# Optimization experiments

Hardware: AMD Instinct MI355X
Metric: run time of the kernel (lower is better)

## Reference

```python
import jax, jax.numpy as jnp
import numpy as np

NB = 5  # frequency bands


def _ln(x, g, b, eps=1e-5):
    m = jnp.mean(x, axis=-1, keepdims=True)
    v = jnp.var(x, axis=-1, keepdims=True)
    return (x - m) / jnp.sqrt(v + eps) * g + b


def _graph_adj(x, adj_w, sw1, sb1, sw2, sb2, pos_factor, pos_enc):
    # x: [B, D, N] -> degree-normalized adjacency [B, N, N]
    d = x.shape[1]
    xt = jnp.swapaxes(x, 1, 2)  # [B, N, D]
    # concat-MLP first layer split: cat(xi, xj) @ W1 == xi @ W1[:d] + xj @ W1[d:]
    a = xt @ sw1[:d]
    bpart = xt @ sw1[d:]
    h = jax.nn.elu(a[:, :, None, :] + bpart[:, None, :, :] + sb1)  # [B, N, N, H]
    dyn = jax.nn.sigmoid(jnp.squeeze(h @ sw2, -1) + sb2)  # [B, N, N]
    static = jax.nn.softmax(adj_w, axis=-1)
    pos = jax.nn.softmax(pos_enc, axis=-1)
    comb = jax.nn.softmax(static + dyn + pos_factor * pos, axis=-1)
    deg = jnp.sum(comb, axis=-1)
    dis = (deg + 1e-8) ** -0.5
    return dis[:, :, None] * comb * dis[:, None, :]


def _gcn(x, adj, w, b):
    # x: [B, D, N], adj: [B, N, N] -> [B, D_out, N]
    xt = jnp.swapaxes(x, 1, 2)
    out = jnp.einsum('bij,bjd->bid', adj, xt) @ w + b
    return jnp.swapaxes(out, 1, 2)


def _mha(x, qkv_w, qkv_b, ow, ob, nh=4):
    B, S, D = x.shape
    dh = D // nh
    q, k, v = jnp.split(x @ qkv_w + qkv_b, 3, axis=-1)
    q = q.reshape(B, S, nh, dh)
    k = k.reshape(B, S, nh, dh)
    v = v.reshape(B, S, nh, dh)
    att = jax.nn.softmax(jnp.einsum('bihd,bjhd->bhij', q, k) / float(np.sqrt(dh)), axis=-1)
    o = jnp.einsum('bhij,bjhd->bihd', att, v).reshape(B, S, D)
    return o @ ow + ob


def setup_inputs():
    key = jax.random.key(0)
    B, D, N = 16, 256, 64
    ks = iter(jax.random.split(key, 40))

    def rn(shape, s=0.05):
        return jax.random.normal(next(ks), shape, dtype=jnp.float32) * s

    eyeN = jnp.eye(N, dtype=jnp.float32)
    return dict(
        feature=jax.random.normal(next(ks), (B, NB * D, 1, N), dtype=jnp.float32),
        l_adj_w=jnp.tile(eyeN[None], (NB, 1, 1)),
        l_sim_w1=rn((NB, 2 * D, D)), l_sim_b1=jnp.zeros((NB, D), jnp.float32),
        l_sim_w2=rn((NB, D, 1)), l_sim_b2=jnp.zeros((NB, 1), jnp.float32),
        l_pos_factor=jnp.full((NB,), 0.5, jnp.float32),
        l_pos_enc=jnp.tile(eyeN[None], (NB, 1, 1)),
        l_gcn_w=rn((NB, D, D)), l_gcn_b=jnp.zeros((NB, D), jnp.float32),
        g_adj_w=jnp.eye(NB, dtype=jnp.float32),
        g_sim_w1=rn((2 * D, D)), g_sim_b1=jnp.zeros((D,), jnp.float32),
        g_sim_w2=rn((D, 1)), g_sim_b2=jnp.zeros((1,), jnp.float32),
        g_pos_factor=jnp.float32(0.5),
        g_pos_enc=jnp.eye(NB, dtype=jnp.float32),
        g_gcn_w=rn((D, D)), g_gcn_b=jnp.zeros((D,), jnp.float32),
        qkv_w=rn((D, 3 * D)), qkv_b=jnp.zeros((3 * D,), jnp.float32),
        attn_ow=rn((D, D)), attn_ob=jnp.zeros((D,), jnp.float32),
        ln1_g=jnp.ones((D,), jnp.float32), ln1_b=jnp.zeros((D,), jnp.float32),
        ln2_g=jnp.ones((D,), jnp.float32), ln2_b=jnp.zeros((D,), jnp.float32),
        mlp_w1=rn((D, 4 * D)), mlp_b1=jnp.zeros((4 * D,), jnp.float32),
        mlp_w2=rn((4 * D, D)), mlp_b2=jnp.zeros((D,), jnp.float32),
        imp_w=rn((NB, N, 1)), imp_b=jnp.zeros((NB, 1), jnp.float32),
    )


def reference(feature, l_adj_w, l_sim_w1, l_sim_b1, l_sim_w2, l_sim_b2,
              l_pos_factor, l_pos_enc, l_gcn_w, l_gcn_b,
              g_adj_w, g_sim_w1, g_sim_b1, g_sim_w2, g_sim_b2,
              g_pos_factor, g_pos_enc, g_gcn_w, g_gcn_b,
              qkv_w, qkv_b, attn_ow, attn_ob,
              ln1_g, ln1_b, ln2_g, ln2_b,
              mlp_w1, mlp_b1, mlp_w2, mlp_b2,
              imp_w, imp_b):
    B = feature.shape[0]
    D = l_gcn_w.shape[-1]
    N = feature.shape[-1]
    # [B, 5*D, 1, N] -> [5, B, D, N] band-major
    x5 = jnp.moveaxis(feature.reshape(B, NB, D, N), 1, 0)
    # per-band local graphs + GCNs (vmapped over the 5 bands)
    local_adj = jax.vmap(_graph_adj)(x5, l_adj_w, l_sim_w1, l_sim_b1,
                                     l_sim_w2, l_sim_b2, l_pos_factor, l_pos_enc)
    local_out = jax.vmap(_gcn)(x5, local_adj, l_gcn_w, l_gcn_b)  # [5, B, D, N]
    scale_nodes = jnp.moveaxis(jnp.mean(local_out, axis=-1), 0, 1)  # [B, 5, D]
    # cross-band attention block (pre: MHA + residual + LN, then MLP + residual + LN)
    attn = _mha(scale_nodes, qkv_w, qkv_b, attn_ow, attn_ob)
    h1 = _ln(scale_nodes + attn, ln1_g, ln1_b)
    mlp = jax.nn.gelu(h1 @ mlp_w1 + mlp_b1, approximate=False) @ mlp_w2 + mlp_b2
    se = _ln(h1 + mlp, ln2_g, ln2_b)  # [B, 5, D]
    # global scale graph over the 5 band nodes
    xg = jnp.swapaxes(se, 1, 2)  # [B, D, 5]
    g_adj = _graph_adj(xg, g_adj_w, g_sim_w1, g_sim_b1, g_sim_w2, g_sim_b2,
                       g_pos_factor, g_pos_enc)
    g_out = jnp.swapaxes(_gcn(xg, g_adj, g_gcn_w, g_gcn_b), 1, 2)  # [B, 5, D]
    # modulate each local band feature by its global scale vector
    enh = local_out * jnp.moveaxis(g_out, 1, 0)[..., None]  # [5, B, D, N]
    # per-band importance projection over channels: [5, B, D, 1]
    out5 = jnp.einsum('kbdn,kno->kbdo', enh, imp_w) + imp_b[:, None, None, :]
    output = jnp.moveaxis(out5, 0, 1).reshape(B, NB * D, 1, 1)
    return output, g_adj, jnp.moveaxis(local_out, 0, 1)
```

## Files before the change

### kernel.cpp

```cpp
#include <hip/hip_runtime.h>
#include <hip/hip_bf16.h>

#define NBANDS 5
#define BATCH  16
#define DIM    256
#define NNODE  64
#define SEQ    5

typedef __hip_bfloat16 bf16;
typedef unsigned short ushort_t;
typedef __attribute__((ext_vector_type(8))) short short8;
typedef __attribute__((ext_vector_type(4))) float float4v;

#define MFMA __builtin_amdgcn_mfma_f32_16x16x32_bf16

__device__ __forceinline__ float bu2f(ushort_t u){
    bf16 h = *reinterpret_cast<bf16*>(&u);
    return __bfloat162float(h);
}
__device__ __forceinline__ ushort_t f2bu(float x){
    bf16 h = __float2bfloat16(x);
    return *reinterpret_cast<ushort_t*>(&h);
}
__device__ __forceinline__ float elu(float v){
    return (v > 0.f) ? v : (__expf(v) - 1.f);
}

__global__ void __launch_bounds__(256) k_head(
    const float* __restrict__ l_adj_w, const float* __restrict__ l_pos_enc,
    const float* __restrict__ l_pf,
    const float* __restrict__ g_adj_w, const float* __restrict__ g_pos_enc,
    const float* __restrict__ g_pf,
    float* __restrict__ sbase, float* __restrict__ gbase,
    const float* __restrict__ w1, const float* __restrict__ gw,
    ushort_t* __restrict__ w1bt, ushort_t* __restrict__ gwbt)
{
    int blk = blockIdx.x;
    int tid = threadIdx.x;
    __shared__ ushort_t tile[64][65];

    if (blk < 80) {
        int r = blk*4 + (tid>>6);
        int k = r >> 6, i = r & 63;
        int t = tid & 63;
        float aw = l_adj_w[(k*NNODE + i)*NNODE + t];
        float pe = l_pos_enc[(k*NNODE + i)*NNODE + t];
        float m1 = aw, m2 = pe;
        for (int o=32;o>0;o>>=1){ m1 = fmaxf(m1, __shfl_xor(m1,o,64)); m2 = fmaxf(m2, __shfl_xor(m2,o,64)); }
        float e1 = __expf(aw-m1), e2 = __expf(pe-m2);
        float s1=e1, s2=e2;
        for (int o=32;o>0;o>>=1){ s1 += __shfl_xor(s1,o,64); s2 += __shfl_xor(s2,o,64); }
        float pf = l_pf[k];
        sbase[(k*NNODE+i)*NNODE + t] = e1/s1 + pf*(e2/s2);
    } else if (blk == 80) {
        if (tid < NBANDS) {
            int i = tid;
            float r1[NBANDS], r2[NBANDS];
            float m1=-1e30f, m2=-1e30f;
            for (int j=0;j<NBANDS;j++){
                r1[j]=g_adj_w[i*NBANDS+j]; r2[j]=g_pos_enc[i*NBANDS+j];
                m1=fmaxf(m1,r1[j]); m2=fmaxf(m2,r2[j]);
            }
            float s1=0.f,s2=0.f;
            for (int j=0;j<NBANDS;j++){ r1[j]=__expf(r1[j]-m1); r2[j]=__expf(r2[j]-m2); s1+=r1[j]; s2+=r2[j]; }
            float pf = g_pf[0];
            for (int j=0;j<NBANDS;j++) gbase[i*NBANDS+j] = r1[j]/s1 + pf*(r2[j]/s2);
        }
    } else {
        int idx = blk - 81;
        int inst = idx >> 4;
        int t = idx & 15;
        int r0 = (t>>2)*64, c0 = (t&3)*64;
        const float* src; ushort_t* dst;
        if (inst < 10){
            int k = inst>>1, half = inst&1;
            src = w1  + ((size_t)k*512 + half*256)*256;
            dst = w1bt+ ((size_t)k*512 + half*256)*256;
        } else {
            int k = inst-10;
            src = gw  + (size_t)k*65536;
            dst = gwbt+ (size_t)k*65536;
        }
        int jj = tid & 63, i4 = tid >> 6;
        for (int p=0;p<16;p++){
            int i = p*4 + i4;
            tile[i][jj] = f2bu(src[(size_t)(r0+i)*256 + c0 + jj]);
        }
        __syncthreads();
        for (int p=0;p<16;p++){
            int i = p*4 + i4;
            dst[(size_t)(c0+i)*256 + r0 + jj] = tile[jj][i];
        }
    }
}

__global__ void __launch_bounds__(512) k_graph(
    const float* __restrict__ feat,
    const ushort_t* __restrict__ w1bt, const float* __restrict__ b1,
    const float* __restrict__ w2, const float* __restrict__ b2arr,
    const float* __restrict__ sbase,
    const ushort_t* __restrict__ gwbt, const float* __restrict__ gb,
    const float* __restrict__ imp_w,
    float* __restrict__ out_local,
    float* __restrict__ scalew4, float* __restrict__ impw4)
{
    int k  = blockIdx.x >> 6;
    int b  = (blockIdx.x >> 2) & 15;
    int iq = blockIdx.x & 3;
    int i0 = iq << 4;
    int tid = threadIdx.x;
    int w = tid >> 6, lane = tid & 63, c16 = lane & 15, quad = lane >> 4;

    __shared__ union {
        ushort_t xtb[64][264];
        ushort_t ab[80][264];
    } U;
    __shared__ ushort_t cs[16][72];
    __shared__ ushort_t ys[16][264];

    const float* src = feat + ((size_t)b*NBANDS + k)*DIM*NNODE;

    #pragma unroll
    for (int u = 0; u < 32; ++u){
        int idx = u*512 + tid;
        U.xtb[idx & 63][idx >> 6] = f2bu(src[idx]);
    }
    __syncthreads();

    int col0 = w*32 + c16;
    int col1 = col0 + 16;

    const ushort_t* Ba = w1bt + (size_t)k*512*DIM;
    const ushort_t* Bb = Ba + 256*DIM;
    float4v z = {0.f,0.f,0.f,0.f};
    float4v aA0=z, aA1=z;
    float4v aB00=z,aB01=z,aB10=z,aB11=z,aB20=z,aB21=z,aB30=z,aB31=z;
    #pragma unroll
    for (int ks = 0; ks < 8; ++ks){
        int ko = ks*32 + quad*8;
        short8 fa = *reinterpret_cast<const short8*>(&U.xtb[i0 + c16][ko]);
        short8 f0 = *reinterpret_cast<const short8*>(&U.xtb[ 0 + c16][ko]);
        short8 f1 = *reinterpret_cast<const short8*>(&U.xtb[16 + c16][ko]);
        short8 f2 = *reinterpret_cast<const short8*>(&U.xtb[32 + c16][ko]);
        short8 f3 = *reinterpret_cast<const short8*>(&U.xtb[48 + c16][ko]);
        short8 wa0 = *reinterpret_cast<const short8*>(Ba + (size_t)col0*DIM + ko);
        short8 wa1 = *reinterpret_cast<const short8*>(Ba + (size_t)col1*DIM + ko);
        short8 wb0 = *reinterpret_cast<const short8*>(Bb + (size_t)col0*DIM + ko);
        short8 wb1 = *reinterpret_cast<const short8*>(Bb + (size_t)col1*DIM + ko);
        aA0  = MFMA(fa, wa0, aA0, 0,0,0);
        aA1  = MFMA(fa, wa1, aA1, 0,0,0);
        aB00 = MFMA(f0, wb0, aB00, 0,0,0);
        aB01 = MFMA(f0, wb1, aB01, 0,0,0);
        aB10 = MFMA(f1, wb0, aB10, 0,0,0);
        aB11 = MFMA(f1, wb1, aB11, 0,0,0);
        aB20 = MFMA(f2, wb0, aB20, 0,0,0);
        aB21 = MFMA(f2, wb1, aB21, 0,0,0);
        aB30 = MFMA(f3, wb0, aB30, 0,0,0);
        aB31 = MFMA(f3, wb1, aB31, 0,0,0);
    }
    __syncthreads();
    {
        float bias0 = b1[k*DIM + col0];
        float bias1 = b1[k*DIM + col1];
        int r0 = quad*4;
        #pragma unroll
        for (int r = 0; r < 4; ++r){
            U.ab[r0 + r][col0]      = f2bu(aA0[r] + bias0);
            U.ab[r0 + r][col1]      = f2bu(aA1[r] + bias1);
            U.ab[16 + r0 + r][col0] = f2bu(aB00[r]);
            U.ab[16 + r0 + r][col1] = f2bu(aB01[r]);
            U.ab[32 + r0 + r][col0] = f2bu(aB10[r]);
            U.ab[32 + r0 + r][col1] = f2bu(aB11[r]);
            U.ab[48 + r0 + r][col0] = f2bu(aB20[r]);
            U.ab[48 + r0 + r][col1] = f2bu(aB21[r]);
            U.ab[64 + r0 + r][col0] = f2bu(aB30[r]);
            U.ab[64 + r0 + r][col1] = f2bu(aB31[r]);
        }
    }
    __syncthreads();

    {
        int il0 = w*2, il1 = w*2 + 1;
        ushort4 a0v = *reinterpret_cast<const ushort4*>(&U.ab[il0][lane*4]);
        ushort4 a1v = *reinterpret_cast<const ushort4*>(&U.ab[il1][lane*4]);
        float4  wv  = *reinterpret_cast<const float4*>(&w2[k*DIM + lane*4]);
        float a00=bu2f(a0v.x), a01=bu2f(a0v.y), a02=bu2f(a0v.z), a03=bu2f(a0v.w);
        float a10=bu2f(a1v.x), a11=bu2f(a1v.y), a12=bu2f(a1v.z), a13=bu2f(a1v.w);
        float acc0 = 0.f, acc1 = 0.f;
        #pragma unroll 4
        for (int j = 0; j < 64; ++j){
            ushort4 bv = *reinterpret_cast<const ushort4*>(&U.ab[16 + j][lane*4]);
            float bx=bu2f(bv.x), by=bu2f(bv.y), bz=bu2f(bv.z), bq=bu2f(bv.w);
            float p0 = elu(a00+bx)*wv.x + elu(a01+by)*wv.y
                     + elu(a02+bz)*wv.z + elu(a03+bq)*wv.w;
            float p1 = elu(a10+bx)*wv.x + elu(a11+by)*wv.y
                     + elu(a12+bz)*wv.z + elu(a13+bq)*wv.w;
            for (int o=32;o>0;o>>=1){ p0 += __shfl_xor(p0,o,64); p1 += __shfl_xor(p1,o,64); }
            acc0 = (lane == j) ? p0 : acc0;
            acc1 = (lane == j) ? p1 : acc1;
        }
        float sb2 = b2arr[k];
        float sg0 = 1.f/(1.f + __expf(-(acc0 + sb2)));
        float sg1 = 1.f/(1.f + __expf(-(acc1 + sb2)));
        float val0 = sbase[(k*NNODE + i0 + il0)*NNODE + lane] + sg0;
        float val1 = sbase[(k*NNODE + i0 + il1)*NNODE + lane] + sg1;
        float m0 = val0, m1 = val1;
        for (int o=32;o>0;o>>=1){ m0 = fmaxf(m0, __shfl_xor(m0,o,64)); m1 = fmaxf(m1, __shfl_xor(m1,o,64)); }
        float e0 = __expf(val0 - m0), e1 = __expf(val1 - m1);
        float s0 = e0, s1 = e1;
        for (int o=32;o>0;o>>=1){ s0 += __shfl_xor(s0,o,64); s1 += __shfl_xor(s1,o,64); }
        cs[il0][lane] = f2bu(e0/s0);
        cs[il1][lane] = f2bu(e1/s1);
    }
    __syncthreads();

    {
        float4v aY0 = z, aY1 = z;
        #pragma unroll
        for (int ks = 0; ks < 2; ++ks){
            int ko = ks*32 + quad*8;
            short8 af = *reinterpret_cast<const short8*>(&cs[c16][ko]);
            const float* f0p = src + (size_t)col0*NNODE + ko;
            const float* f1p = src + (size_t)col1*NNODE + ko;
            float4 x0 = *reinterpret_cast<const float4*>(f0p);
            float4 x1 = *reinterpret_cast<const float4*>(f0p+4);
            float4 y0 = *reinterpret_cast<const float4*>(f1p);
            float4 y1 = *reinterpret_cast<const float4*>(f1p+4);
            short8 bf0, bf1;
            bf0[0]=(short)f2bu(x0.x); bf0[1]=(short)f2bu(x0.y); bf0[2]=(short)f2bu(x0.z); bf0[3]=(short)f2bu(x0.w);
            bf0[4]=(short)f2bu(x1.x); bf0[5]=(short)f2bu(x1.y); bf0[6]=(short)f2bu(x1.z); bf0[7]=(short)f2bu(x1.w);
            bf1[0]=(short)f2bu(y0.x); bf1[1]=(short)f2bu(y0.y); bf1[2]=(short)f2bu(y0.z); bf1[3]=(short)f2bu(y0.w);
            bf1[4]=(short)f2bu(y1.x); bf1[5]=(short)f2bu(y1.y); bf1[6]=(short)f2bu(y1.z); bf1[7]=(short)f2bu(y1.w);
            aY0 = MFMA(af, bf0, aY0, 0,0,0);
            aY1 = MFMA(af, bf1, aY1, 0,0,0);
        }
        #pragma unroll
        for (int r=0;r<4;++r){
            ys[quad*4 + r][col0] = f2bu(aY0[r]);
            ys[quad*4 + r][col1] = f2bu(aY1[r]);
        }
    }
    __syncthreads();

    {
        float4v aG0 = z, aG1 = z;
        const ushort_t* Bg = gwbt + (size_t)k*DIM*DIM;
        #pragma unroll
        for (int ks = 0; ks < 8; ++ks){
            int ko = ks*32 + quad*8;
            short8 af = *reinterpret_cast<const short8*>(&ys[c16][ko]);
            short8 g0 = *reinterpret_cast<const short8*>(Bg + (size_t)col0*DIM + ko);
            short8 g1 = *reinterpret_cast<const short8*>(Bg + (size_t)col1*DIM + ko);
            aG0 = MFMA(af, g0, aG0, 0,0,0);
            aG1 = MFMA(af, g1, aG1, 0,0,0);
        }
        int nb = i0 + quad*4;
        float iw0 = imp_w[k*NNODE + nb + 0];
        float iw1 = imp_w[k*NNODE + nb + 1];
        float iw2 = imp_w[k*NNODE + nb + 2];
        float iw3 = imp_w[k*NNODE + nb + 3];
        size_t obase = ((size_t)b*NBANDS + k)*DIM;

        float bias0 = gb[k*DIM + col0];
        float v0 = aG0[0]+bias0, v1 = aG0[1]+bias0, v2 = aG0[2]+bias0, v3 = aG0[3]+bias0;
        float4 vv = make_float4(v0,v1,v2,v3);
        *reinterpret_cast<float4*>(&out_local[(obase + col0)*NNODE + nb]) = vv;
        float s  = v0+v1+v2+v3;
        float di = v0*iw0 + v1*iw1 + v2*iw2 + v3*iw3;
        s  += __shfl_xor(s,16,64);  s  += __shfl_xor(s,32,64);
        di += __shfl_xor(di,16,64); di += __shfl_xor(di,32,64);
        if (quad == 0){
            size_t o = ((size_t)iq*80 + b*SEQ + k)*DIM + col0;
            scalew4[o] = s;
            impw4[o]   = di;
        }

        float bias1 = gb[k*DIM + col1];
        v0 = aG1[0]+bias1; v1 = aG1[1]+bias1; v2 = aG1[2]+bias1; v3 = aG1[3]+bias1;
        vv = make_float4(v0,v1,v2,v3);
        *reinterpret_cast<float4*>(&out_local[(obase + col1)*NNODE + nb]) = vv;
        s  = v0+v1+v2+v3;
        di = v0*iw0 + v1*iw1 + v2*iw2 + v3*iw3;
        s  += __shfl_xor(s,16,64);  s  += __shfl_xor(s,32,64);
        di += __shfl_xor(di,16,64); di += __shfl_xor(di,32,64);
        if (quad == 0){
            size_t o = ((size_t)iq*80 + b*SEQ + k)*DIM + col1;
            scalew4[o] = s;
            impw4[o]   = di;
        }
    }
}

__global__ void __launch_bounds__(256) k_qkv_gemv(const float* __restrict__ scalew4,
                        const float* __restrict__ w, const float* __restrict__ bias,
                        float* __restrict__ out)
{
    int row = blockIdx.x / 12;
    int n0 = (blockIdx.x % 12) * 64;
    int tid = threadIdx.x;
    int c = tid & 63, s = tid >> 6;
    __shared__ float xs[DIM];
    __shared__ float part[4][64];
    {
        size_t basei = (size_t)row*DIM + tid;
        xs[tid] = (scalew4[basei] + scalew4[20480 + basei]
                 + scalew4[40960 + basei] + scalew4[61440 + basei]) * (1.f/64.f);
    }
    __syncthreads();
    const float* wp = w + (size_t)(s*64)*768 + n0 + c;
    const float* xp = xs + s*64;
    float acc = 0.f;
    #pragma unroll 8
    for (int i = 0; i < 64; ++i) acc += xp[i] * wp[(size_t)i*768];
    part[s][c] = acc;
    __syncthreads();
    if (s == 0){
        out[(size_t)row*768 + n0 + c] = bias[n0+c] + part[0][c]+part[1][c]+part[2][c]+part[3][c];
    }
}

template<int COLS, int SLICES>
__global__ void __launch_bounds__(256) k_gemv(const float* __restrict__ x, const float* __restrict__ w,
                       const float* __restrict__ bias, float* __restrict__ out,
                       int K, int N, int act)
{
    int chunks = N / COLS;
    int row = blockIdx.x / chunks;
    int n0 = (blockIdx.x % chunks) * COLS;
    int c = threadIdx.x % COLS, s = threadIdx.x / COLS;
    __shared__ float xs[1024];
    __shared__ float part[SLICES][COLS];
    for (int i = threadIdx.x; i < K; i += 256) xs[i] = x[(size_t)row*K + i];
    __syncthreads();
    int klen = K / SLICES;
    const float* wp = w + (size_t)(s*klen)*N + n0 + c;
    const float* xp = xs + s*klen;
    float acc = 0.f;
    #pragma unroll 8
    for (int i = 0; i < klen; ++i) acc += xp[i] * wp[(size_t)i*N];
    part[s][c] = acc;
    __syncthreads();
    if (s == 0){
        float v = bias[n0+c];
        #pragma unroll
        for (int q=0;q<SLICES;q++) v += part[q][c];
        if (act) v = 0.5f*v*(1.f + erff(v*0.70710678118654752f));
        out[(size_t)row*N + n0 + c] = v;
    }
}

__global__ void __launch_bounds__(256) k_projattn(const float* __restrict__ qkvw,
                        const float* __restrict__ ow, const float* __restrict__ ob,
                        float* __restrict__ projw)
{
    int row = blockIdx.x / 4;
    int n0 = (blockIdx.x % 4) * 64;
    int b = row / SEQ, i = row % SEQ;
    int tid = threadIdx.x;
    int h = tid >> 6, l = tid & 63;
    __shared__ float xs[DIM];
    __shared__ float part[4][64];
    const float* base = qkvw + (size_t)b*SEQ*3*DIM;
    float qv = base[(size_t)i*3*DIM + h*64 + l];
    float pj[SEQ];
    #pragma unroll
    for (int j=0;j<SEQ;j++){
        float p = qv * base[(size_t)j*3*DIM + DIM + h*64 + l];
        for (int o=32;o>0;o>>=1) p += __shfl_xor(p,o,64);
        pj[j] = p * 0.125f;
    }
    float m = pj[0];
    #pragma unroll
    for (int j=1;j<SEQ;j++) m = fmaxf(m, pj[j]);
    float ssum = 0.f;
    #pragma unroll
    for (int j=0;j<SEQ;j++){ pj[j] = __expf(pj[j]-m); ssum += pj[j]; }
    float inv = 1.f/ssum;
    float o = 0.f;
    #pragma unroll
    for (int j=0;j<SEQ;j++) o += pj[j]*inv * base[(size_t)j*3*DIM + 2*DIM + h*64 + l];
    xs[tid] = o;
    __syncthreads();
    int c = tid & 63, s = tid >> 6;
    const float* wp = ow + (size_t)(s*64)*DIM + n0 + c;
    const float* xp = xs + s*64;
    float acc = 0.f;
    #pragma unroll 8
    for (int k=0;k<64;++k) acc += xp[k] * wp[(size_t)k*DIM];
    part[s][c] = acc;
    __syncthreads();
    if (s == 0){
        projw[(size_t)row*DIM + n0 + c] = ob[n0+c] + part[0][c]+part[1][c]+part[2][c]+part[3][c];
    }
}

__device__ __forceinline__ float block_ln(float v, int tid, float* red, float g, float bln)
{
    float s = v;
    for (int o=32;o>0;o>>=1) s += __shfl_xor(s,o,64);
    int wave = tid>>6, lane = tid&63;
    if (lane==0) red[wave] = s;
    __syncthreads();
    float mean = (red[0]+red[1]+red[2]+red[3]) * (1.f/DIM);
    float c = v - mean;
    float q = c*c;
    for (int o=32;o>0;o>>=1) q += __shfl_xor(q,o,64);
    __syncthreads();
    if (lane==0) red[wave] = q;
    __syncthreads();
    float var = (red[0]+red[1]+red[2]+red[3]) * (1.f/DIM);
    return c * rsqrtf(var + 1e-5f) * g + bln;
}

__global__ void __launch_bounds__(256) k_mlp1_ln(const float* __restrict__ projw,
                         const float* __restrict__ scalew4,
                         const float* __restrict__ ln1_g, const float* __restrict__ ln1_b,
                         const float* __restrict__ w1, const float* __restrict__ b1,
                         float* __restrict__ h1w, float* __restrict__ mhw)
{
    int row = blockIdx.x / 16;
    int n0 = (blockIdx.x % 16) * 64;
    int tid = threadIdx.x;
    __shared__ float xs[DIM];
    __shared__ float red[4];
    __shared__ float part[4][64];
    size_t basei = (size_t)row*DIM + tid;
    float sc = (scalew4[basei] + scalew4[20480 + basei]
              + scalew4[40960 + basei] + scalew4[61440 + basei]) * (1.f/64.f);
    float v = projw[basei] + sc;
    float h = block_ln(v, tid, red, ln1_g[tid], ln1_b[tid]);
    xs[tid] = h;
    if ((blockIdx.x % 16) == 0) h1w[basei] = h;
    __syncthreads();
    int c = tid & 63, s = tid >> 6;
    const float* wp = w1 + (size_t)(s*64)*1024 + n0 + c;
    const float* xp = xs + s*64;
    float acc = 0.f;
    #pragma unroll 8
    for (int i=0;i<64;++i) acc += xp[i] * wp[(size_t)i*1024];
    part[s][c] = acc;
    __syncthreads();
    if (s == 0){
        float o = b1[n0+c] + part[0][c] + part[1][c] + part[2][c] + part[3][c];
        o = 0.5f*o*(1.f + erff(o*0.70710678118654752f));
        mhw[(size_t)row*1024 + n0 + c] = o;
    }
}

__global__ void __launch_bounds__(256) k_gab_ln(const float* __restrict__ m2w,
                        const float* __restrict__ h1w,
                        const float* __restrict__ ln2_g, const float* __restrict__ ln2_b,
                        const float* __restrict__ gw1, const float* __restrict__ gb1,
                        float* __restrict__ sew, float* __restrict__ gaw, float* __restrict__ gbw)
{
    int row = blockIdx.x / 4;
    int n0 = (blockIdx.x % 4) * 64;
    int tid = threadIdx.x;
    __shared__ float xs[DIM];
    __shared__ float red[4];
    __shared__ float partA[4][64];
    __shared__ float partB[4][64];
    float v = m2w[(size_t)row*DIM + tid] + h1w[(size_t)row*DIM + tid];
    float h = block_ln(v, tid, red, ln2_g[tid], ln2_b[tid]);
    xs[tid] = h;
    if ((blockIdx.x % 4) == 0) sew[(size_t)row*DIM + tid] = h;
    __syncthreads();
    int c = tid & 63, s = tid >> 6;
    const float* wpA = gw1 + (size_t)(s*64)*DIM + n0 + c;
    const float* wpB = wpA + (size_t)DIM*DIM;
    const float* xp = xs + s*64;
    float aA = 0.f, aB = 0.f;
    #pragma unroll 8
    for (int i=0;i<64;++i){
        float xv = xp[i];
        aA += xv * wpA[(size_t)i*DIM];
        aB += xv * wpB[(size_t)i*DIM];
    }
    partA[s][c] = aA;
    partB[s][c] = aB;
    __syncthreads();
    if (s == 0){
        gaw[(size_t)row*DIM + n0 + c] = gb1[n0+c] + partA[0][c]+partA[1][c]+partA[2][c]+partA[3][c];
        gbw[(size_t)row*DIM + n0 + c] = partB[0][c]+partB[1][c]+partB[2][c]+partB[3][c];
    }
}

__global__ void __launch_bounds__(256) k_goutfin(const float* __restrict__ gaw,
                        const float* __restrict__ gbw,
                        const float* __restrict__ gw2, const float* __restrict__ gb2,
                        const float* __restrict__ gbase,
                        const float* __restrict__ sew,
                        const float* __restrict__ ggw, const float* __restrict__ ggb,
                        const float* __restrict__ impw4, const float* __restrict__ imp_b,
                        float* __restrict__ out0, float* __restrict__ out_gadj)
{
    int row = blockIdx.x / 4;
    int n0 = (blockIdx.x % 4) * 64;
    int b = row / SEQ, i = row % SEQ;
    int tid = threadIdx.x;
    int wave = tid >> 6, lane = tid & 63;
    __shared__ float dyn_s[SEQ];
    __shared__ float xs[DIM];
    __shared__ float part[4][64];
    for (int j = wave; j < SEQ; j += 4){
        const float* gar = gaw + (size_t)row*DIM;
        const float* gbr = gbw + ((size_t)b*SEQ + j)*DIM;
        float acc = 0.f;
        #pragma unroll
        for (int m=0;m<4;m++){
            int dd = lane + m*64;
            float v = gar[dd] + gbr[dd];
            acc += elu(v) * gw2[dd];
        }
        for (int o=32;o>0;o>>=1) acc += __shfl_xor(acc,o,64);
        if (lane==0) dyn_s[j] = acc;
    }
    __syncthreads();
    float gc[SEQ];
    {
        float sb2 = gb2[0];
        float m = -1e30f;
        #pragma unroll
        for (int j=0;j<SEQ;j++){
            float sg = 1.f/(1.f+__expf(-(dyn_s[j]+sb2)));
            gc[j] = gbase[i*SEQ+j] + sg;
            m = fmaxf(m, gc[j]);
        }
        float ssum=0.f;
        #pragma unroll
        for (int j=0;j<SEQ;j++){ gc[j]=__expf(gc[j]-m); ssum+=gc[j]; }
        float inv = 1.f/ssum;
        #pragma unroll
        for (int j=0;j<SEQ;j++) gc[j] *= inv;
    }
    if (n0 == 0 && tid < SEQ) out_gadj[((size_t)b*SEQ+i)*SEQ + tid] = gc[tid];
    float t = 0.f;
    #pragma unroll
    for (int j=0;j<SEQ;j++) t += gc[j]*sew[((size_t)b*SEQ + j)*DIM + tid];
    xs[tid] = t;
    __syncthreads();
    int c = tid & 63, s = tid >> 6;
    const float* wp = ggw + (size_t)(s*64)*DIM + n0 + c;
    const float* xp = xs + s*64;
    float acc = 0.f;
    #pragma unroll 8
    for (int k=0;k<64;++k) acc += xp[k] * wp[(size_t)k*DIM];
    part[s][c] = acc;
    __syncthreads();
    if (s == 0){
        float g = ggb[n0+c] + part[0][c]+part[1][c]+part[2][c]+part[3][c];
        size_t o = (size_t)row*DIM + n0 + c;
        float imps = impw4[o] + impw4[20480 + o] + impw4[40960 + o] + impw4[61440 + o];
        out0[o] = g * imps + imp_b[i];
    }
}

extern "C" void kernel_launch(void* const* d_in, const int* in_sizes, int n_in,
                              void* d_out, int out_size, void* d_ws, size_t ws_size,
                              hipStream_t stream)
{
    const float* feature      = (const float*)d_in[0];
    const float* l_adj_w      = (const float*)d_in[1];
    const float* l_sim_w1     = (const float*)d_in[2];
    const float* l_sim_b1     = (const float*)d_in[3];
    const float* l_sim_w2     = (const float*)d_in[4];
    const float* l_sim_b2     = (const float*)d_in[5];
    const float* l_pos_factor = (const float*)d_in[6];
    const float* l_pos_enc    = (const float*)d_in[7];
    const float* l_gcn_w      = (const float*)d_in[8];
    const float* l_gcn_b      = (const float*)d_in[9];
    const float* g_adj_w      = (const float*)d_in[10];
    const float* g_sim_w1     = (const float*)d_in[11];
    const float* g_sim_b1     = (const float*)d_in[12];
    const float* g_sim_w2     = (const float*)d_in[13];
    const float* g_sim_b2     = (const float*)d_in[14];
    const float* g_pos_factor = (const float*)d_in[15];
    const float* g_pos_enc    = (const float*)d_in[16];
    const float* g_gcn_w      = (const float*)d_in[17];
    const float* g_gcn_b      = (const float*)d_in[18];
    const float* qkv_w        = (const float*)d_in[19];
    const float* qkv_b        = (const float*)d_in[20];
    const float* attn_ow      = (const float*)d_in[21];
    const float* attn_ob      = (const float*)d_in[22];
    const float* ln1_g        = (const float*)d_in[23];
    const float* ln1_b        = (const float*)d_in[24];
    const float* ln2_g        = (const float*)d_in[25];
    const float* ln2_b        = (const float*)d_in[26];
    const float* mlp_w1       = (const float*)d_in[27];
    const float* mlp_b1      = (const float*)d_in[28];
    const float* mlp_w2       = (const float*)d_in[29];
    const float* mlp_b2       = (const float*)d_in[30];
    const float* imp_w        = (const float*)d_in[31];
    const float* imp_b        = (const float*)d_in[32];

    float* out0      = (float*)d_out;
    float* out_gadj  = out0 + (size_t)BATCH*NBANDS*DIM;
    float* out_local = out_gadj + (size_t)BATCH*NBANDS*NBANDS;

    ushort_t* w1bt = (ushort_t*)d_ws;
    ushort_t* gwbt = w1bt + (size_t)NBANDS*512*DIM;
    float* fp = (float*)(gwbt + (size_t)NBANDS*DIM*DIM);
    float* sbase   = fp; fp += NBANDS*NNODE*NNODE;
    float* gbase   = fp; fp += 32;
    float* scalew4 = fp; fp += 4*BATCH*SEQ*DIM;
    float* impw4   = fp; fp += 4*BATCH*SEQ*DIM;
    float* qkvw    = fp; fp += BATCH*SEQ*3*DIM;
    float* projw   = fp; fp += BATCH*SEQ*DIM;
    float* h1w     = fp; fp += BATCH*SEQ*DIM;
    float* mhw     = fp; fp += BATCH*SEQ*4*DIM;
    float* m2w     = fp; fp += BATCH*SEQ*DIM;
    float* sew     = fp; fp += BATCH*SEQ*DIM;
    float* gaw     = fp; fp += BATCH*SEQ*DIM;
    float* gbw     = fp; fp += BATCH*SEQ*DIM;

    const int ROWS = BATCH*SEQ;

    k_head<<<321, 256, 0, stream>>>(l_adj_w, l_pos_enc, l_pos_factor,
                                    g_adj_w, g_pos_enc, g_pos_factor,
                                    sbase, gbase,
                                    l_sim_w1, l_gcn_w, w1bt, gwbt);
    k_graph<<<NBANDS*BATCH*4, 512, 0, stream>>>(feature, w1bt, l_sim_b1,
                                    l_sim_w2, l_sim_b2, sbase,
                                    gwbt, l_gcn_b, imp_w,
                                    out_local, scalew4, impw4);
    k_qkv_gemv<<<ROWS*12, 256, 0, stream>>>(scalew4, qkv_w, qkv_b, qkvw);
    k_projattn<<<ROWS*4, 256, 0, stream>>>(qkvw, attn_ow, attn_ob, projw);
    k_mlp1_ln<<<ROWS*16, 256, 0, stream>>>(projw, scalew4, ln1_g, ln1_b, mlp_w1, mlp_b1, h1w, mhw);
    k_gemv<32,8><<<ROWS*8, 256, 0, stream>>>(mhw, mlp_w2, mlp_b2, m2w, 1024, 256, 0);
    k_gab_ln<<<ROWS*4, 256, 0, stream>>>(m2w, h1w, ln2_g, ln2_b, g_sim_w1, g_sim_b1, sew, gaw, gbw);
    k_goutfin<<<ROWS*4, 256, 0, stream>>>(gaw, gbw, g_sim_w2, g_sim_b2, gbase,
                                          sew, g_gcn_w, g_gcn_b, impw4, imp_b,
                                          out0, out_gadj);
}
```

Before: 228.7 us.

## Give each lane its own node j in the pairwise MLP to drop per-j shuffle reductions

The dynamic-adjacency inner loop used to split the hidden dimension across lanes and needed a 64-lane butterfly reduction for every neighbour j. Now each lane owns one j and loops over the hidden dimension serially. To support this, the b-part tile is stored with a padded stride of 266 to avoid LDS bank conflicts, w2 is staged in shared memory, and the a-part gets its own buffer. The block order is also remapped so the four i-quarters sharing a (band, batch) are spread across the grid, and the sbase/bias loads are hoisted before the first barrier. The cost is more shared memory per block and more serial arithmetic per lane.

```diff
diff --git a/kernel.cpp b/kernel.cpp
--- a/kernel.cpp
+++ b/kernel.cpp
@@ -104,26 +104,32 @@
     float* __restrict__ out_local,
     float* __restrict__ scalew4, float* __restrict__ impw4)
 {
-    int k  = blockIdx.x >> 6;
-    int b  = (blockIdx.x >> 2) & 15;
-    int iq = blockIdx.x & 3;
+    int kb = blockIdx.x % 80;
+    int iq = blockIdx.x / 80;
+    int k  = kb >> 4;
+    int b  = kb & 15;
     int i0 = iq << 4;
     int tid = threadIdx.x;
     int w = tid >> 6, lane = tid & 63, c16 = lane & 15, quad = lane >> 4;
 
-    __shared__ union {
-        ushort_t xtb[64][264];
-        ushort_t ab[80][264];
-    } U;
+    __shared__ ushort_t Ubuf[64*266 + 8];
+    __shared__ ushort_t as[16][264];
     __shared__ ushort_t cs[16][72];
     __shared__ ushort_t ys[16][264];
+    __shared__ float w2s[DIM];
 
     const float* src = feat + ((size_t)b*NBANDS + k)*DIM*NNODE;
 
+    int il0 = w*2, il1 = w*2 + 1;
+    float sb0 = sbase[(k*NNODE + i0 + il0)*NNODE + lane];
+    float sb1 = sbase[(k*NNODE + i0 + il1)*NNODE + lane];
+    float sbias2 = b2arr[k];
+
+    if (tid < DIM) w2s[tid] = w2[k*DIM + tid];
     #pragma unroll
     for (int u = 0; u < 32; ++u){
         int idx = u*512 + tid;
-        U.xtb[idx & 63][idx >> 6] = f2bu(src[idx]);
+        Ubuf[(idx & 63)*264 + (idx >> 6)] = f2bu(src[idx]);
     }
     __syncthreads();
 
@@ -138,11 +144,11 @@
     #pragma unroll
     for (int ks = 0; ks < 8; ++ks){
         int ko = ks*32 + quad*8;
-        short8 fa = *reinterpret_cast<const short8*>(&U.xtb[i0 + c16][ko]);
-        short8 f0 = *reinterpret_cast<const short8*>(&U.xtb[ 0 + c16][ko]);
-        short8 f1 = *reinterpret_cast<const short8*>(&U.xtb[16 + c16][ko]);
-        short8 f2 = *reinterpret_cast<const short8*>(&U.xtb[32 + c16][ko]);
-        short8 f3 = *reinterpret_cast<const short8*>(&U.xtb[48 + c16][ko]);
+        short8 fa = *reinterpret_cast<const short8*>(&Ubuf[(i0 + c16)*264 + ko]);
+        short8 f0 = *reinterpret_cast<const short8*>(&Ubuf[( 0 + c16)*264 + ko]);
+        short8 f1 = *reinterpret_cast<const short8*>(&Ubuf[(16 + c16)*264 + ko]);
+        short8 f2 = *reinterpret_cast<const short8*>(&Ubuf[(32 + c16)*264 + ko]);
+        short8 f3 = *reinterpret_cast<const short8*>(&Ubuf[(48 + c16)*264 + ko]);
         short8 wa0 = *reinterpret_cast<const short8*>(Ba + (size_t)col0*DIM + ko);
         short8 wa1 = *reinterpret_cast<const short8*>(Ba + (size_t)col1*DIM + ko);
         short8 wb0 = *reinterpret_cast<const short8*>(Bb + (size_t)col0*DIM + ko);
@@ -165,45 +171,45 @@
         int r0 = quad*4;
         #pragma unroll
         for (int r = 0; r < 4; ++r){
-            U.ab[r0 + r][col0]      = f2bu(aA0[r] + bias0);
-            U.ab[r0 + r][col1]      = f2bu(aA1[r] + bias1);
-            U.ab[16 + r0 + r][col0] = f2bu(aB00[r]);
-            U.ab[16 + r0 + r][col1] = f2bu(aB01[r]);
-            U.ab[32 + r0 + r][col0] = f2bu(aB10[r]);
-            U.ab[32 + r0 + r][col1] = f2bu(aB11[r]);
-            U.ab[48 + r0 + r][col0] = f2bu(aB20[r]);
-            U.ab[48 + r0 + r][col1] = f2bu(aB21[r]);
-            U.ab[64 + r0 + r][col0] = f2bu(aB30[r]);
-            U.ab[64 + r0 + r][col1] = f2bu(aB31[r]);
+            as[r0 + r][col0] = f2bu(aA0[r] + bias0);
+            as[r0 + r][col1] = f2bu(aA1[r] + bias1);
+            Ubuf[( 0 + r0 + r)*266 + col0] = f2bu(aB00[r]);
+            Ubuf[( 0 + r0 + r)*266 + col1] = f2bu(aB01[r]);
+            Ubuf[(16 + r0 + r)*266 + col0] = f2bu(aB10[r]);
+            Ubuf[(16 + r0 + r)*266 + col1] = f2bu(aB11[r]);
+            Ubuf[(32 + r0 + r)*266 + col0] = f2bu(aB20[r]);
+            Ubuf[(32 + r0 + r)*266 + col1] = f2bu(aB21[r]);
+            Ubuf[(48 + r0 + r)*266 + col0] = f2bu(aB30[r]);
+            Ubuf[(48 + r0 + r)*266 + col1] = f2bu(aB31[r]);
         }
     }
     __syncthreads();
 
     {
-        int il0 = w*2, il1 = w*2 + 1;
-        ushort4 a0v = *reinterpret_cast<const ushort4*>(&U.ab[il0][lane*4]);
-        ushort4 a1v = *reinterpret_cast<const ushort4*>(&U.ab[il1][lane*4]);
-        float4  wv  = *reinterpret_cast<const float4*>(&w2[k*DIM + lane*4]);
-        float a00=bu2f(a0v.x), a01=bu2f(a0v.y), a02=bu2f(a0v.z), a03=bu2f(a0v.w);
-        float a10=bu2f(a1v.x), a11=bu2f(a1v.y), a12=bu2f(a1v.z), a13=bu2f(a1v.w);
+        const ushort_t* bd = Ubuf + 266*lane;
+        const ushort_t* a0p = as[il0];
+        const ushort_t* a1p = as[il1];
         float acc0 = 0.f, acc1 = 0.f;
         #pragma unroll 4
-        for (int j = 0; j < 64; ++j){
-            ushort4 bv = *reinterpret_cast<const ushort4*>(&U.ab[16 + j][lane*4]);
-            float bx=bu2f(bv.x), by=bu2f(bv.y), bz=bu2f(bv.z), bq=bu2f(bv.w);
-            float p0 = elu(a00+bx)*wv.x + elu(a01+by)*wv.y
-                     + elu(a02+bz)*wv.z + elu(a03+bq)*wv.w;
-            float p1 = elu(a10+bx)*wv.x + elu(a11+by)*wv.y
-                     + elu(a12+bz)*wv.z + elu(a13+bq)*wv.w;
-            for (int o=32;o>0;o>>=1){ p0 += __shfl_xor(p0,o,64); p1 += __shfl_xor(p1,o,64); }
-            acc0 = (lane == j) ? p0 : acc0;
-            acc1 = (lane == j) ? p1 : acc1;
-        }
-        float sb2 = b2arr[k];
-        float sg0 = 1.f/(1.f + __expf(-(acc0 + sb2)));
-        float sg1 = 1.f/(1.f + __expf(-(acc1 + sb2)));
-        float val0 = sbase[(k*NNODE + i0 + il0)*NNODE + lane] + sg0;
-        float val1 = sbase[(k*NNODE + i0 + il1)*NNODE + lane] + sg1;
+        for (int dd = 0; dd < 64; ++dd){
+            unsigned int blo = *reinterpret_cast<const unsigned int*>(bd + dd*4);
+            unsigned int bhi = *reinterpret_cast<const unsigned int*>(bd + dd*4 + 2);
+            ushort4 a0 = *reinterpret_cast<const ushort4*>(a0p + dd*4);
+            ushort4 a1 = *reinterpret_cast<const ushort4*>(a1p + dd*4);
+            float4 wv  = *reinterpret_cast<const float4*>(&w2s[dd*4]);
+            float bx = bu2f((ushort_t)(blo & 0xffffu));
+            float by = bu2f((ushort_t)(blo >> 16));
+            float bz = bu2f((ushort_t)(bhi & 0xffffu));
+            float bq = bu2f((ushort_t)(bhi >> 16));
+            acc0 += elu(bu2f(a0.x)+bx)*wv.x + elu(bu2f(a0.y)+by)*wv.y
+                  + elu(bu2f(a0.z)+bz)*wv.z + elu(bu2f(a0.w)+bq)*wv.w;
+            acc1 += elu(bu2f(a1.x)+bx)*wv.x + elu(bu2f(a1.y)+by)*wv.y
+                  + elu(bu2f(a1.z)+bz)*wv.z + elu(bu2f(a1.w)+bq)*wv.w;
+        }
+        float sg0 = 1.f/(1.f + __expf(-(acc0 + sbias2)));
+        float sg1 = 1.f/(1.f + __expf(-(acc1 + sbias2)));
+        float val0 = sb0 + sg0;
+        float val1 = sb1 + sg1;
         float m0 = val0, m1 = val1;
         for (int o=32;o>0;o>>=1){ m0 = fmaxf(m0, __shfl_xor(m0,o,64)); m1 = fmaxf(m1, __shfl_xor(m1,o,64)); }
         float e0 = __expf(val0 - m0), e1 = __expf(val1 - m1);
@@ -214,8 +220,8 @@
     }
     __syncthreads();
 
+    float4v aY0 = z, aY1 = z;
     {
-        float4v aY0 = z, aY1 = z;
         #pragma unroll
         for (int ks = 0; ks < 2; ++ks){
             int ko = ks*32 + quad*8;
@@ -587,7 +593,7 @@
     const float* ln2_g        = (const float*)d_in[25];
     const float* ln2_b        = (const float*)d_in[26];
     const float* mlp_w1       = (const float*)d_in[27];
-    const float* mlp_b1      = (const float*)d_in[28];
+    const float* mlp_b1       = (const float*)d_in[28];
     const float* mlp_w2       = (const float*)d_in[29];
     const float* mlp_b2       = (const float*)d_in[30];
     const float* imp_w        = (const float*)d_in[31];
```

Measured after the change: 215.8 us. 1.06x faster.
